# Optimization experiments

Hardware: AMD Instinct MI355X
Metric: run time of the kernel (lower is better)

## Reference

```python
import jax, jax.numpy as jnp
import numpy as np

DIM = 128  # feature dim, used for 1/sqrt(dim) scaling


def setup_inputs() -> dict:
    key = jax.random.key(0)
    kq, kk, kv, kpq, kpk = jax.random.split(key, 5)
    B, S, D = 16, 2048, DIM
    return {
        "Q": jax.random.normal(kq, (B, S, D), dtype=jnp.float32),
        "K": jax.random.normal(kk, (B, S, D), dtype=jnp.float32),
        "V": jax.random.normal(kv, (B, S, D), dtype=jnp.float32),
        "p_q": jax.random.uniform(kpq, (B, S, 1), dtype=jnp.float32),
        "p_k": jax.random.uniform(kpk, (B, S, 1), dtype=jnp.float32),
    }


def reference(Q, K, V, p_q, p_k):
    # A: [B, Sq, Sk] scaled dot-product scores
    scale = 1.0 / jnp.sqrt(jnp.asarray(DIM, dtype=Q.dtype))
    A = jnp.einsum("bqd,bkd->bqk", Q, K) * scale
    # multiplicative pre-gate: p_q [B,Sq,1] * p_k^T [B,1,Sk]
    A = A * p_q * jnp.swapaxes(p_k, -2, -1)
    W = jax.nn.softmax(A, axis=-1)
    return jnp.einsum("bqk,bkd->bqd", W, V)
```

## Files before the change

kernel.cpp:

```cpp
#include <hip/hip_runtime.h>
#include <hip/hip_fp16.h>


typedef _Float16 f16x8 __attribute__((ext_vector_type(8)));
typedef float f32x16 __attribute__((ext_vector_type(16)));
typedef unsigned int u32x4 __attribute__((ext_vector_type(4)));

#define S_LEN 2048
#define DD 128
#define TILE_BYTES 16384
#define NT 32

#define EXP2(x) __builtin_amdgcn_exp2f(x)

__device__ __forceinline__ unsigned int pk2(float a, float b) {
  __half2 h = __float22half2_rn(make_float2(a, b));
  return __builtin_bit_cast(unsigned int, h);
}

__device__ __forceinline__ void st8(void* dst, const float v[8]) {
  u32x4 u;
  u[0] = pk2(v[0], v[1]);
  u[1] = pk2(v[2], v[3]);
  u[2] = pk2(v[4], v[5]);
  u[3] = pk2(v[6], v[7]);
  *(u32x4*)dst = u;
}

__device__ __forceinline__ void gld16(const void* g, void* l) {
  __builtin_amdgcn_global_load_lds(
      (const __attribute__((address_space(1))) unsigned int*)g,
      (__attribute__((address_space(3))) unsigned int*)l, 16, 0, 0);
}

__global__ __launch_bounds__(256) void prep_q_k(const float* __restrict__ Q,
                                                const float* __restrict__ pq,
                                                char* __restrict__ qh) {
  size_t i = ((size_t)blockIdx.x * 256 + threadIdx.x) * 8;
  const float g = pq[i >> 7] * 0.12751743343158394f;
  float4 a = *(const float4*)(Q + i);
  float4 b = *(const float4*)(Q + i + 4);
  float v[8] = {a.x * g, a.y * g, a.z * g, a.w * g,
                b.x * g, b.y * g, b.z * g, b.w * g};
  st8(qh + i * 2, v);
}

__global__ __launch_bounds__(256) void prep_kv(
    const float* __restrict__ K, const float* __restrict__ V,
    const float* __restrict__ pk, char* __restrict__ kimg,
    char* __restrict__ vimg) {
  __shared__ float vt[64 * 132];
  const int t = threadIdx.x;
  const int bid = blockIdx.x;
  const int bq = bid & 15;
  const int kt = bid >> 4;
  const size_t rowbase = (size_t)bq * S_LEN + kt * 64;

#pragma unroll
  for (int cc = 0; cc < 8; ++cc) {
    const int f = cc * 256 + t;
    const int row = f >> 5;
    const int col = (f & 31) * 4;
    *(float4*)(vt + row * 132 + col) = *(const float4*)(V + (rowbase + row) * DD + col);
  }

  char* kdst = kimg + (size_t)(bq * NT + kt) * TILE_BYTES;
#pragma unroll
  for (int cc = 0; cc < 4; ++cc) {
    const int p0 = (cc * 256 + t) * 16;
    const int key = p0 >> 8;
    const int d0 = ((p0 & 255) ^ ((key & 7) << 4)) >> 1;
    const float g = pk[rowbase + key];
    const float* src = K + (rowbase + key) * DD + d0;
    float4 a = *(const float4*)(src);
    float4 b = *(const float4*)(src + 4);
    float v[8] = {a.x * g, a.y * g, a.z * g, a.w * g,
                  b.x * g, b.y * g, b.z * g, b.w * g};
    st8(kdst + p0, v);
  }

  __syncthreads();

  char* vdst = vimg + (size_t)(bq * NT + kt) * TILE_BYTES;
#pragma unroll
  for (int cc = 0; cc < 4; ++cc) {
    const int p0 = (cc * 256 + t) * 16;
    const int dcol = p0 >> 7;
    const int key0 = ((p0 & 127) ^ ((dcol & 7) << 4)) >> 1;
    float v[8];
#pragma unroll
    for (int j = 0; j < 8; ++j) v[j] = vt[(key0 + j) * 132 + dcol];
    st8(vdst + p0, v);
  }
}

__global__ __launch_bounds__(256, 2) void attn_main(const char* __restrict__ qh,
                                                    const char* __restrict__ kimg,
                                                    const char* __restrict__ vimg,
                                                    float* __restrict__ out) {
  __shared__ float4 ldsraw[4160];
  char* lds = (char*)ldsraw;
  const int tid = threadIdx.x;
  const int wid = tid >> 6;
  const int qs = wid >> 1;
  const int ks = wid & 1;
  const int lane = tid & 63;
  const int c = lane & 31;
  const int h = lane >> 5;
  const int swz = (c & 7) << 4;
  const int bid = blockIdx.x;
  const int bq = 2 * (bid & 7) + ((bid >> 3) & 1);
  const int qt = bid >> 4;
  const int q0 = qt * 64 + qs * 32;

  f16x8 qf[8];
  const char* qrow = qh + (size_t)(bq * S_LEN + q0 + c) * (DD * 2);
#pragma unroll
  for (int kc = 0; kc < 8; ++kc) qf[kc] = *(const f16x8*)(qrow + kc * 32 + h * 16);

  f32x16 acc[4];
#pragma unroll
  for (int d = 0; d < 4; ++d) {
#pragma unroll
    for (int r = 0; r < 16; ++r) acc[d][r] = 0.f;
  }
  float m_run = -1.0e30f, l_run = 0.f;

  const char* kb = kimg + (size_t)bq * (NT * TILE_BYTES);
  const char* vb = vimg + (size_t)bq * (NT * TILE_BYTES);

#pragma unroll
  for (int j = 0; j < 4; ++j) {
    gld16(kb + j * 4096 + tid * 16, lds + j * 4096 + tid * 16);
    gld16(vb + j * 4096 + tid * 16, lds + TILE_BYTES + j * 4096 + tid * 16);
  }

  for (int kt = 0; kt < NT; ++kt) {
    __syncthreads();
    const int cur = (kt & 1) << 15;
    if (kt + 1 < NT) {
      const int nxt = ((kt + 1) & 1) << 15;
      const char* kn = kb + (size_t)(kt + 1) * TILE_BYTES;
      const char* vn = vb + (size_t)(kt + 1) * TILE_BYTES;
#pragma unroll
      for (int j = 0; j < 4; ++j) {
        gld16(kn + j * 4096 + tid * 16, lds + nxt + j * 4096 + tid * 16);
        gld16(vn + j * 4096 + tid * 16, lds + nxt + TILE_BYTES + j * 4096 + tid * 16);
      }
    }
    const char* kl = lds + cur;
    const char* vl = lds + cur + TILE_BYTES;

    f32x16 sa, sb;
#pragma unroll
    for (int r = 0; r < 16; ++r) { sa[r] = 0.f; sb[r] = 0.f; }
    __builtin_amdgcn_s_setprio(1);
#pragma unroll
    for (int kc = 0; kc < 4; ++kc) {
      f16x8 kfa = *(const f16x8*)(kl + (ks * 32 + c) * 256 + ((kc * 32 + h * 16) ^ swz));
      f16x8 kfb = *(const f16x8*)(kl + (ks * 32 + c) * 256 + (((kc + 4) * 32 + h * 16) ^ swz));
      sa = __builtin_amdgcn_mfma_f32_32x32x16_f16(kfa, qf[kc], sa, 0, 0, 0);
      sb = __builtin_amdgcn_mfma_f32_32x32x16_f16(kfb, qf[kc + 4], sb, 0, 0, 0);
    }
    __builtin_amdgcn_s_setprio(0);
    f32x16 s;
#pragma unroll
    for (int r = 0; r < 16; ++r) s[r] = sa[r] + sb[r];

    float m0 = fmaxf(s[0], s[1]), m1 = fmaxf(s[2], s[3]);
    float m2 = fmaxf(s[4], s[5]), m3 = fmaxf(s[6], s[7]);
    float m4 = fmaxf(s[8], s[9]), m5 = fmaxf(s[10], s[11]);
    float m6 = fmaxf(s[12], s[13]), m7 = fmaxf(s[14], s[15]);
    m0 = fmaxf(m0, m1); m2 = fmaxf(m2, m3); m4 = fmaxf(m4, m5); m6 = fmaxf(m6, m7);
    float cm = fmaxf(fmaxf(m0, m2), fmaxf(m4, m6));
    cm = fmaxf(cm, __shfl_xor(cm, 32));
    if (__any(cm > m_run + 11.0f)) {
      const float mn = fmaxf(m_run, cm);
      const float al = EXP2(m_run - mn);
      m_run = mn;
      l_run *= al;
#pragma unroll
      for (int d = 0; d < 4; ++d) {
#pragma unroll
        for (int r = 0; r < 16; ++r) acc[d][r] *= al;
      }
    }
    float ps0 = 0.f, ps1 = 0.f;
#pragma unroll
    for (int r = 0; r < 8; ++r) {
      s[r] = EXP2(s[r] - m_run);       ps0 += s[r];
      s[r + 8] = EXP2(s[r + 8] - m_run); ps1 += s[r + 8];
    }
    l_run += ps0 + ps1;

#pragma unroll
    for (int kc = 0; kc < 2; ++kc) {
      const int A = kc * 8;
      const int Bb = A + 4;
      unsigned pA0 = pk2(s[A + 0], s[A + 1]);
      unsigned pA1 = pk2(s[A + 2], s[A + 3]);
      unsigned pB0 = pk2(s[Bb + 0], s[Bb + 1]);
      unsigned pB1 = pk2(s[Bb + 2], s[Bb + 3]);
      unsigned own0 = h ? pB0 : pA0;
      unsigned own1 = h ? pB1 : pA1;
      unsigned snd0 = h ? pA0 : pB0;
      unsigned snd1 = h ? pA1 : pB1;
      unsigned rcv0 = __shfl_xor(snd0, 32);
      unsigned rcv1 = __shfl_xor(snd1, 32);
      u32x4 pw;
      pw[0] = h ? rcv0 : own0;
      pw[1] = h ? rcv1 : own1;
      pw[2] = h ? own0 : rcv0;
      pw[3] = h ? own1 : rcv1;
      f16x8 pf = __builtin_bit_cast(f16x8, pw);
      const int kci = ks * 2 + kc;
      __builtin_amdgcn_s_setprio(1);
#pragma unroll
      for (int d = 0; d < 4; ++d) {
        f16x8 vf = *(const f16x8*)(vl + (d * 32 + c) * 128 + ((kci * 32 + h * 16) ^ swz));
        acc[d] = __builtin_amdgcn_mfma_f32_32x32x16_f16(vf, pf, acc[d], 0, 0, 0);
      }
      __builtin_amdgcn_s_setprio(0);
    }
  }

  l_run += __shfl_xor(l_run, 32);

  __syncthreads();
  float2* ml = (float2*)(lds + 65536);
  if (h == 0) ml[wid * 32 + c] = make_float2(m_run, l_run);
  __syncthreads();
  const float2 po = ml[(wid ^ 1) * 32 + c];
  const float ms = fmaxf(m_run, po.x);
  const float lstar = l_run * EXP2(m_run - ms) + po.y * EXP2(po.x - ms);
  const float w = EXP2(m_run - ms) / lstar;

  char* T = lds;
  if (ks == 0) {
#pragma unroll
    for (int d = 0; d < 4; ++d) {
#pragma unroll
      for (int rr = 0; rr < 4; ++rr) {
        const int dd = d * 32 + rr * 8 + h * 4;
        float4 v4;
        v4.x = acc[d][rr * 4 + 0] * w;
        v4.y = acc[d][rr * 4 + 1] * w;
        v4.z = acc[d][rr * 4 + 2] * w;
        v4.w = acc[d][rr * 4 + 3] * w;
        *(float4*)(T + (qs * 32 + c) * 512 + ((dd * 4) ^ swz)) = v4;
      }
    }
  }
  __syncthreads();
  if (ks == 1) {
#pragma unroll
    for (int d = 0; d < 4; ++d) {
#pragma unroll
      for (int rr = 0; rr < 4; ++rr) {
        const int dd = d * 32 + rr * 8 + h * 4;
        float4* p = (float4*)(T + (qs * 32 + c) * 512 + ((dd * 4) ^ swz));
        float4 t = *p;
        t.x += acc[d][rr * 4 + 0] * w;
        t.y += acc[d][rr * 4 + 1] * w;
        t.z += acc[d][rr * 4 + 2] * w;
        t.w += acc[d][rr * 4 + 3] * w;
        *p = t;
      }
    }
  }
  __syncthreads();

  float* obase = out + ((size_t)bq * S_LEN + qt * 64) * DD;
#pragma unroll
  for (int p = 0; p < 8; ++p) {
    const int idx = p * 256 + tid;
    const int q = idx >> 5;
    const int d0 = (idx & 31) * 4;
    float4 v4 = *(const float4*)(T + q * 512 + ((d0 * 4) ^ ((q & 7) << 4)));
    *(float4*)(obase + q * DD + d0) = v4;
  }
}

extern "C" void kernel_launch(void* const* d_in, const int* in_sizes, int n_in,
                              void* d_out, int out_size, void* d_ws, size_t ws_size,
                              hipStream_t stream) {
  const float* Q = (const float*)d_in[0];
  const float* K = (const float*)d_in[1];
  const float* V = (const float*)d_in[2];
  const float* pq = (const float*)d_in[3];
  const float* pk = (const float*)d_in[4];
  float* out = (float*)d_out;
  char* ws = (char*)d_ws;
  char* qh = ws;
  char* kimg = ws + (8u << 20);
  char* vimg = ws + (16u << 20);

  prep_q_k<<<2048, 256, 0, stream>>>(Q, pq, qh);
  prep_kv<<<512, 256, 0, stream>>>(K, V, pk, kimg, vimg);
  attn_main<<<512, 256, 0, stream>>>(qh, kimg, vimg, out);
}
```

Before: 71.47 us.

## Fuse Q prep into attention, give each wave full key tile, pre-swizzle fragments

Drops the separate Q conversion kernel and converts Q to scaled fp16 inside the attention kernel. Each block now covers 128 queries, with each of its four waves owning 32 queries across all 64 keys of a tile, so the cross-wave softmax merge and two-pass output reduction go away. The K/V tile images are rebuilt in MFMA fragment order so LDS reads become contiguous without XOR swizzle. The grid halves to 256 blocks, which may underfill the 256 CUs at two blocks per CU, and each wave now does twice the matmul work per tile.

```diff
diff --git a/kernel.cpp b/kernel.cpp
--- a/kernel.cpp
+++ b/kernel.cpp
@@ -31,18 +31,6 @@
   __builtin_amdgcn_global_load_lds(
       (const __attribute__((address_space(1))) unsigned int*)g,
       (__attribute__((address_space(3))) unsigned int*)l, 16, 0, 0);
-}
-
-__global__ __launch_bounds__(256) void prep_q_k(const float* __restrict__ Q,
-                                                const float* __restrict__ pq,
-                                                char* __restrict__ qh) {
-  size_t i = ((size_t)blockIdx.x * 256 + threadIdx.x) * 8;
-  const float g = pq[i >> 7] * 0.12751743343158394f;
-  float4 a = *(const float4*)(Q + i);
-  float4 b = *(const float4*)(Q + i + 4);
-  float v[8] = {a.x * g, a.y * g, a.z * g, a.w * g,
-                b.x * g, b.y * g, b.z * g, b.w * g};
-  st8(qh + i * 2, v);
 }
 
 __global__ __launch_bounds__(256) void prep_kv(
@@ -67,16 +55,20 @@
   char* kdst = kimg + (size_t)(bq * NT + kt) * TILE_BYTES;
 #pragma unroll
   for (int cc = 0; cc < 4; ++cc) {
-    const int p0 = (cc * 256 + t) * 16;
-    const int key = p0 >> 8;
-    const int d0 = ((p0 & 255) ^ ((key & 7) << 4)) >> 1;
+    const int i = cc * 256 + t;
+    const int cI = i & 31;
+    const int ksub = (i >> 5) & 1;
+    const int hI = (i >> 6) & 1;
+    const int kcI = i >> 7;
+    const int key = ksub * 32 + cI;
+    const int d0 = kcI * 16 + hI * 8;
     const float g = pk[rowbase + key];
     const float* src = K + (rowbase + key) * DD + d0;
     float4 a = *(const float4*)(src);
     float4 b = *(const float4*)(src + 4);
     float v[8] = {a.x * g, a.y * g, a.z * g, a.w * g,
                   b.x * g, b.y * g, b.z * g, b.w * g};
-    st8(kdst + p0, v);
+    st8(kdst + i * 16, v);
   }
 
   __syncthreads();
@@ -84,47 +76,36 @@
   char* vdst = vimg + (size_t)(bq * NT + kt) * TILE_BYTES;
 #pragma unroll
   for (int cc = 0; cc < 4; ++cc) {
-    const int p0 = (cc * 256 + t) * 16;
-    const int dcol = p0 >> 7;
-    const int key0 = ((p0 & 127) ^ ((dcol & 7) << 4)) >> 1;
+    const int i = cc * 256 + t;
+    const int cI = i & 31;
+    const int dI = (i >> 5) & 3;
+    const int hI = (i >> 7) & 1;
+    const int kcI = i >> 8;
+    const int key0 = kcI * 16 + hI * 8;
+    const int dcol = dI * 32 + cI;
     float v[8];
 #pragma unroll
-    for (int j = 0; j < 8; ++j) v[j] = vt[(key0 + j) * 132 + dcol];
-    st8(vdst + p0, v);
-  }
-}
-
-__global__ __launch_bounds__(256, 2) void attn_main(const char* __restrict__ qh,
+    for (int e = 0; e < 8; ++e) v[e] = vt[(key0 + e) * 132 + dcol];
+    st8(vdst + i * 16, v);
+  }
+}
+
+__global__ __launch_bounds__(256, 2) void attn_main(const float* __restrict__ Q,
+                                                    const float* __restrict__ pq,
                                                     const char* __restrict__ kimg,
                                                     const char* __restrict__ vimg,
                                                     float* __restrict__ out) {
-  __shared__ float4 ldsraw[4160];
+  __shared__ float4 ldsraw[4096];
   char* lds = (char*)ldsraw;
   const int tid = threadIdx.x;
   const int wid = tid >> 6;
-  const int qs = wid >> 1;
-  const int ks = wid & 1;
   const int lane = tid & 63;
   const int c = lane & 31;
   const int h = lane >> 5;
-  const int swz = (c & 7) << 4;
   const int bid = blockIdx.x;
   const int bq = 2 * (bid & 7) + ((bid >> 3) & 1);
   const int qt = bid >> 4;
-  const int q0 = qt * 64 + qs * 32;
-
-  f16x8 qf[8];
-  const char* qrow = qh + (size_t)(bq * S_LEN + q0 + c) * (DD * 2);
-#pragma unroll
-  for (int kc = 0; kc < 8; ++kc) qf[kc] = *(const f16x8*)(qrow + kc * 32 + h * 16);
-
-  f32x16 acc[4];
-#pragma unroll
-  for (int d = 0; d < 4; ++d) {
-#pragma unroll
-    for (int r = 0; r < 16; ++r) acc[d][r] = 0.f;
-  }
-  float m_run = -1.0e30f, l_run = 0.f;
+  const int q0 = qt * 128 + wid * 32;
 
   const char* kb = kimg + (size_t)bq * (NT * TILE_BYTES);
   const char* vb = vimg + (size_t)bq * (NT * TILE_BYTES);
@@ -134,6 +115,30 @@
     gld16(kb + j * 4096 + tid * 16, lds + j * 4096 + tid * 16);
     gld16(vb + j * 4096 + tid * 16, lds + TILE_BYTES + j * 4096 + tid * 16);
   }
+
+  const size_t qgrow = (size_t)bq * S_LEN + q0 + c;
+  const float g = pq[qgrow] * 0.12751743343158394f;
+  const float* qsrc = Q + qgrow * DD;
+  f16x8 qf[8];
+#pragma unroll
+  for (int kc = 0; kc < 8; ++kc) {
+    float4 a = *(const float4*)(qsrc + kc * 16 + h * 8);
+    float4 b = *(const float4*)(qsrc + kc * 16 + h * 8 + 4);
+    u32x4 u;
+    u[0] = pk2(a.x * g, a.y * g);
+    u[1] = pk2(a.z * g, a.w * g);
+    u[2] = pk2(b.x * g, b.y * g);
+    u[3] = pk2(b.z * g, b.w * g);
+    qf[kc] = __builtin_bit_cast(f16x8, u);
+  }
+
+  f32x16 acc[4];
+#pragma unroll
+  for (int d = 0; d < 4; ++d) {
+#pragma unroll
+    for (int r = 0; r < 16; ++r) acc[d][r] = 0.f;
+  }
+  float m_run = -1.0e30f, l_run = 0.f;
 
   for (int kt = 0; kt < NT; ++kt) {
     __syncthreads();
@@ -148,29 +153,29 @@
         gld16(vn + j * 4096 + tid * 16, lds + nxt + TILE_BYTES + j * 4096 + tid * 16);
       }
     }
-    const char* kl = lds + cur;
-    const char* vl = lds + cur + TILE_BYTES;
-
-    f32x16 sa, sb;
-#pragma unroll
-    for (int r = 0; r < 16; ++r) { sa[r] = 0.f; sb[r] = 0.f; }
+
+    const char* kA = lds + cur + h * 1024 + c * 16;
+    f32x16 s0, s1;
+#pragma unroll
+    for (int r = 0; r < 16; ++r) { s0[r] = 0.f; s1[r] = 0.f; }
     __builtin_amdgcn_s_setprio(1);
 #pragma unroll
-    for (int kc = 0; kc < 4; ++kc) {
-      f16x8 kfa = *(const f16x8*)(kl + (ks * 32 + c) * 256 + ((kc * 32 + h * 16) ^ swz));
-      f16x8 kfb = *(const f16x8*)(kl + (ks * 32 + c) * 256 + (((kc + 4) * 32 + h * 16) ^ swz));
-      sa = __builtin_amdgcn_mfma_f32_32x32x16_f16(kfa, qf[kc], sa, 0, 0, 0);
-      sb = __builtin_amdgcn_mfma_f32_32x32x16_f16(kfb, qf[kc + 4], sb, 0, 0, 0);
+    for (int kc = 0; kc < 8; ++kc) {
+      f16x8 k0 = *(const f16x8*)(kA + kc * 2048);
+      f16x8 k1 = *(const f16x8*)(kA + kc * 2048 + 512);
+      s0 = __builtin_amdgcn_mfma_f32_32x32x16_f16(k0, qf[kc], s0, 0, 0, 0);
+      s1 = __builtin_amdgcn_mfma_f32_32x32x16_f16(k1, qf[kc], s1, 0, 0, 0);
     }
     __builtin_amdgcn_s_setprio(0);
-    f32x16 s;
-#pragma unroll
-    for (int r = 0; r < 16; ++r) s[r] = sa[r] + sb[r];
-
-    float m0 = fmaxf(s[0], s[1]), m1 = fmaxf(s[2], s[3]);
-    float m2 = fmaxf(s[4], s[5]), m3 = fmaxf(s[6], s[7]);
-    float m4 = fmaxf(s[8], s[9]), m5 = fmaxf(s[10], s[11]);
-    float m6 = fmaxf(s[12], s[13]), m7 = fmaxf(s[14], s[15]);
+
+    float m0 = fmaxf(fmaxf(s0[0], s0[1]), fmaxf(s0[2], s0[3]));
+    float m1 = fmaxf(fmaxf(s0[4], s0[5]), fmaxf(s0[6], s0[7]));
+    float m2 = fmaxf(fmaxf(s0[8], s0[9]), fmaxf(s0[10], s0[11]));
+    float m3 = fmaxf(fmaxf(s0[12], s0[13]), fmaxf(s0[14], s0[15]));
+    float m4 = fmaxf(fmaxf(s1[0], s1[1]), fmaxf(s1[2], s1[3]));
+    float m5 = fmaxf(fmaxf(s1[4], s1[5]), fmaxf(s1[6], s1[7]));
+    float m6 = fmaxf(fmaxf(s1[8], s1[9]), fmaxf(s1[10], s1[11]));
+    float m7 = fmaxf(fmaxf(s1[12], s1[13]), fmaxf(s1[14], s1[15]));
     m0 = fmaxf(m0, m1); m2 = fmaxf(m2, m3); m4 = fmaxf(m4, m5); m6 = fmaxf(m6, m7);
     float cm = fmaxf(fmaxf(m0, m2), fmaxf(m4, m6));
     cm = fmaxf(cm, __shfl_xor(cm, 32));
@@ -185,22 +190,22 @@
         for (int r = 0; r < 16; ++r) acc[d][r] *= al;
       }
     }
-    float ps0 = 0.f, ps1 = 0.f;
-#pragma unroll
-    for (int r = 0; r < 8; ++r) {
-      s[r] = EXP2(s[r] - m_run);       ps0 += s[r];
-      s[r + 8] = EXP2(s[r + 8] - m_run); ps1 += s[r + 8];
-    }
-    l_run += ps0 + ps1;
-
-#pragma unroll
-    for (int kc = 0; kc < 2; ++kc) {
-      const int A = kc * 8;
-      const int Bb = A + 4;
-      unsigned pA0 = pk2(s[A + 0], s[A + 1]);
-      unsigned pA1 = pk2(s[A + 2], s[A + 3]);
-      unsigned pB0 = pk2(s[Bb + 0], s[Bb + 1]);
-      unsigned pB1 = pk2(s[Bb + 2], s[Bb + 3]);
+
+    const char* vA = lds + cur + TILE_BYTES + h * 2048 + c * 16;
+    float ps = 0.f;
+#pragma unroll
+    for (int kc = 0; kc < 4; ++kc) {
+      const f32x16 pn = (kc < 2) ? s0 : s1;
+      const int A = (kc & 1) * 8;
+      float e0 = EXP2(pn[A + 0] - m_run), e1 = EXP2(pn[A + 1] - m_run);
+      float e2 = EXP2(pn[A + 2] - m_run), e3 = EXP2(pn[A + 3] - m_run);
+      float e4 = EXP2(pn[A + 4] - m_run), e5 = EXP2(pn[A + 5] - m_run);
+      float e6 = EXP2(pn[A + 6] - m_run), e7 = EXP2(pn[A + 7] - m_run);
+      ps += ((e0 + e1) + (e2 + e3)) + ((e4 + e5) + (e6 + e7));
+      unsigned pA0 = pk2(e0, e1);
+      unsigned pA1 = pk2(e2, e3);
+      unsigned pB0 = pk2(e4, e5);
+      unsigned pB1 = pk2(e6, e7);
       unsigned own0 = h ? pB0 : pA0;
       unsigned own1 = h ? pB1 : pA1;
       unsigned snd0 = h ? pA0 : pB0;
@@ -213,66 +218,41 @@
       pw[2] = h ? own0 : rcv0;
       pw[3] = h ? own1 : rcv1;
       f16x8 pf = __builtin_bit_cast(f16x8, pw);
-      const int kci = ks * 2 + kc;
       __builtin_amdgcn_s_setprio(1);
 #pragma unroll
       for (int d = 0; d < 4; ++d) {
-        f16x8 vf = *(const f16x8*)(vl + (d * 32 + c) * 128 + ((kci * 32 + h * 16) ^ swz));
+        f16x8 vf = *(const f16x8*)(vA + kc * 4096 + d * 512);
         acc[d] = __builtin_amdgcn_mfma_f32_32x32x16_f16(vf, pf, acc[d], 0, 0, 0);
       }
       __builtin_amdgcn_s_setprio(0);
     }
+    l_run += ps;
   }
 
   l_run += __shfl_xor(l_run, 32);
+  const float w = 1.0f / l_run;
 
   __syncthreads();
-  float2* ml = (float2*)(lds + 65536);
-  if (h == 0) ml[wid * 32 + c] = make_float2(m_run, l_run);
+  const int swz = (c & 7) << 4;
+  char* T = lds;
+#pragma unroll
+  for (int d = 0; d < 4; ++d) {
+#pragma unroll
+    for (int rr = 0; rr < 4; ++rr) {
+      const int dd = d * 32 + rr * 8 + h * 4;
+      float4 v4;
+      v4.x = acc[d][rr * 4 + 0] * w;
+      v4.y = acc[d][rr * 4 + 1] * w;
+      v4.z = acc[d][rr * 4 + 2] * w;
+      v4.w = acc[d][rr * 4 + 3] * w;
+      *(float4*)(T + (wid * 32 + c) * 512 + ((dd * 4) ^ swz)) = v4;
+    }
+  }
   __syncthreads();
-  const float2 po = ml[(wid ^ 1) * 32 + c];
-  const float ms = fmaxf(m_run, po.x);
-  const float lstar = l_run * EXP2(m_run - ms) + po.y * EXP2(po.x - ms);
-  const float w = EXP2(m_run - ms) / lstar;
-
-  char* T = lds;
-  if (ks == 0) {
-#pragma unroll
-    for (int d = 0; d < 4; ++d) {
-#pragma unroll
-      for (int rr = 0; rr < 4; ++rr) {
-        const int dd = d * 32 + rr * 8 + h * 4;
-        float4 v4;
-        v4.x = acc[d][rr * 4 + 0] * w;
-        v4.y = acc[d][rr * 4 + 1] * w;
-        v4.z = acc[d][rr * 4 + 2] * w;
-        v4.w = acc[d][rr * 4 + 3] * w;
-        *(float4*)(T + (qs * 32 + c) * 512 + ((dd * 4) ^ swz)) = v4;
-      }
-    }
-  }
-  __syncthreads();
-  if (ks == 1) {
-#pragma unroll
-    for (int d = 0; d < 4; ++d) {
-#pragma unroll
-      for (int rr = 0; rr < 4; ++rr) {
-        const int dd = d * 32 + rr * 8 + h * 4;
-        float4* p = (float4*)(T + (qs * 32 + c) * 512 + ((dd * 4) ^ swz));
-        float4 t = *p;
-        t.x += acc[d][rr * 4 + 0] * w;
-        t.y += acc[d][rr * 4 + 1] * w;
-        t.z += acc[d][rr * 4 + 2] * w;
-        t.w += acc[d][rr * 4 + 3] * w;
-        *p = t;
-      }
-    }
-  }
-  __syncthreads();
-
-  float* obase = out + ((size_t)bq * S_LEN + qt * 64) * DD;
-#pragma unroll
-  for (int p = 0; p < 8; ++p) {
+
+  float* obase = out + ((size_t)bq * S_LEN + qt * 128) * DD;
+#pragma unroll
+  for (int p = 0; p < 16; ++p) {
     const int idx = p * 256 + tid;
     const int q = idx >> 5;
     const int d0 = (idx & 31) * 4;
@@ -291,11 +271,9 @@
   const float* pk = (const float*)d_in[4];
   float* out = (float*)d_out;
   char* ws = (char*)d_ws;
-  char* qh = ws;
-  char* kimg = ws + (8u << 20);
-  char* vimg = ws + (16u << 20);
-
-  prep_q_k<<<2048, 256, 0, stream>>>(Q, pq, qh);
+  char* kimg = ws;
+  char* vimg = ws + (8u << 20);
+
   prep_kv<<<512, 256, 0, stream>>>(K, V, pk, kimg, vimg);
-  attn_main<<<512, 256, 0, stream>>>(qh, kimg, vimg, out);
-}
+  attn_main<<<256, 256, 0, stream>>>(Q, pq, kimg, vimg, out);
+}
```

Result: faster. 67.91 us (-5.0%).
